# Performance work log

Measured on AMD Instinct MI355X. Metric: run time of the kernel, lower is better.

Reference implementation:

```python
import jax, jax.numpy as jnp
import numpy as np

B, C, H, W = 4, 256, 64, 64
CI = C // 2
EPS = 1e-5


def setup_inputs() -> dict:
    key = jax.random.key(0)
    ks = jax.random.split(key, 3)
    return {
        "x": jax.random.normal(ks[0], (B, C, H, W), dtype=jnp.float32) * 0.1,
        "g_w": jax.random.normal(ks[1], (CI, C), dtype=jnp.float32) * 0.05,
        "g_b": jnp.zeros((CI,), dtype=jnp.float32),
        "W_w": jax.random.normal(ks[2], (C, CI), dtype=jnp.float32) * 0.05,
        "W_b": jnp.zeros((C,), dtype=jnp.float32),
        "gamma": jnp.ones((C,), dtype=jnp.float32),
        "beta": jnp.zeros((C,), dtype=jnp.float32),
    }


def reference(x, g_w, g_b, W_w, W_b, gamma, beta):
    b, c, h, w = x.shape
    n = h * w
    ci = g_w.shape[0]
    # g: 1x1 conv C -> C/2
    g_x = jnp.einsum('oc,bchw->bohw', g_w, x) + g_b[None, :, None, None]
    g_x = g_x.reshape(b, ci, n).transpose(0, 2, 1)          # [B, N, Ci]
    theta = x.reshape(b, c, n).transpose(0, 2, 1)           # [B, N, C]
    phi = x.reshape(b, c, n)                                # [B, C, N]
    f = jnp.einsum('bnc,bcm->bnm', theta, phi)              # [B, N, N]
    attn = jax.nn.softmax(f, axis=-1)
    y = jnp.einsum('bnm,bmc->bnc', attn, g_x)               # [B, N, Ci]
    y = y.transpose(0, 2, 1).reshape(b, ci, h, w)
    # W: 1x1 conv C/2 -> C, then BatchNorm2d (training-mode batch stats)
    wy = jnp.einsum('oc,bchw->bohw', W_w, y) + W_b[None, :, None, None]
    mean = wy.mean(axis=(0, 2, 3))
    var = wy.var(axis=(0, 2, 3))  # biased, as torch BN uses for normalization
    wy = (wy - mean[None, :, None, None]) * jax.lax.rsqrt(var[None, :, None, None] + EPS)
    wy = wy * gamma[None, :, None, None] + beta[None, :, None, None]
    return wy + x
```

## Files before the change

kernel.cpp:

```cpp
#include <hip/hip_runtime.h>
#include <math.h>

#define B_ 4
#define C_ 256
#define CI_ 128
#define N_ 4096
#define QT_ 128
#define KT_ 64
#define KH_ 2048
#define NITER (KH_ / KT_)
#define KSTRIDE 264
#define VSTRIDE 72
constexpr float EPS_ = 1e-5f;

typedef __attribute__((ext_vector_type(8))) short bfrag;
typedef __attribute__((ext_vector_type(4))) float f4;

__device__ __forceinline__ unsigned short bf16r(float x) {
    unsigned u = __float_as_uint(x);
    u += 0x7FFFu + ((u >> 16) & 1u);
    return (unsigned short)(u >> 16);
}
__device__ __forceinline__ unsigned pack_bf16(float a, float b) {
    unsigned ua = __float_as_uint(a); ua += 0x7FFFu + ((ua >> 16) & 1u);
    unsigned ub = __float_as_uint(b); ub += 0x7FFFu + ((ub >> 16) & 1u);
    return (ua >> 16) | (ub & 0xFFFF0000u);
}

__global__ __launch_bounds__(256) void make_xt(const float* __restrict__ x,
                                               unsigned short* __restrict__ xt,
                                               float* __restrict__ sums) {
    if (blockIdx.x == 0 && blockIdx.y == 0 && blockIdx.z == 0) {
        sums[threadIdx.x] = 0.f;
        sums[threadIdx.x + 256] = 0.f;
    }
    int n  = blockIdx.x * 256 + threadIdx.x;
    int c0 = blockIdx.y * 8;
    int b  = blockIdx.z;
    const float* xb = x + (size_t)b * C_ * N_;
    unsigned short buf[8];
#pragma unroll
    for (int c = 0; c < 8; c++) buf[c] = bf16r(xb[(c0 + c) * N_ + n]);
    uint4 v;
    v.x = buf[0] | ((unsigned)buf[1] << 16);
    v.y = buf[2] | ((unsigned)buf[3] << 16);
    v.z = buf[4] | ((unsigned)buf[5] << 16);
    v.w = buf[6] | ((unsigned)buf[7] << 16);
    *(uint4*)&xt[((size_t)b * N_ + n) * C_ + c0] = v;
}

__global__ __launch_bounds__(256) void gconv(const float* __restrict__ x,
                                             const float* __restrict__ gw,
                                             const float* __restrict__ gb,
                                             unsigned short* __restrict__ gx) {
    int m  = blockIdx.x * 256 + threadIdx.x;
    int o0 = blockIdx.y * 16;
    int b  = blockIdx.z;
    const float* xb = x + (size_t)b * C_ * N_;
    float acc[16];
#pragma unroll
    for (int o = 0; o < 16; o++) acc[o] = gb[o0 + o];
    for (int c0 = 0; c0 < C_; c0 += 8) {
        float xv[8];
#pragma unroll
        for (int j = 0; j < 8; j++) xv[j] = xb[(c0 + j) * N_ + m];
#pragma unroll
        for (int o = 0; o < 16; o++) {
            const float* wr = gw + (size_t)(o0 + o) * C_ + c0;
#pragma unroll
            for (int j = 0; j < 8; j++) acc[o] += wr[j] * xv[j];
        }
    }
#pragma unroll
    for (int o = 0; o < 16; o++)
        gx[((size_t)b * CI_ + o0 + o) * N_ + m] = bf16r(acc[o]);
}

__global__ __launch_bounds__(1024, 4) void attn(const unsigned short* __restrict__ xt,
                                                const unsigned short* __restrict__ gx,
                                                float* __restrict__ Yp,
                                                float* __restrict__ ml) {
    __shared__ __align__(16) unsigned short Ks[2][64 * KSTRIDE];
    __shared__ __align__(16) unsigned short Vs[2][128 * VSTRIDE];
    __shared__ __align__(16) unsigned short Ps[128 * VSTRIDE];

    const int tid  = threadIdx.x;
    const int lane = tid & 63, w = tid >> 6;
    const int wq = w & 7, g = w >> 3;
    const int quad = lane >> 4, ql = lane & 15;
    const int half = blockIdx.x & 1;
    const int b    = (blockIdx.x & 7) >> 1;
    const int qt   = blockIdx.x >> 3;
    const int n0   = qt * QT_;
    const int kbase = half * KH_;
    const unsigned short* xtb = xt + (size_t)b * N_ * C_;
    const unsigned short* gxb = gx + (size_t)b * CI_ * N_;

    bfrag qb[8];
#pragma unroll
    for (int ks = 0; ks < 8; ks++)
        qb[ks] = *(const bfrag*)(xtb + (size_t)(n0 + 16 * wq + ql) * C_ + 32 * ks + quad * 8);

    f4 yacc[8];
    const f4 zero4 = {0.f, 0.f, 0.f, 0.f};
#pragma unroll
    for (int i = 0; i < 8; i++) yacc[i] = zero4;
    float mrun = -INFINITY, lrun = 0.f;

    uint4 kreg[2], vreg[1];
#pragma unroll
    for (int r = 0; r < 2; r++) {
        int idx = r * 1024 + tid;
        kreg[r] = *(const uint4*)(xtb + (size_t)(kbase + (idx >> 5)) * C_ + (idx & 31) * 8);
    }
    vreg[0] = *(const uint4*)(gxb + (size_t)(tid >> 3) * N_ + kbase + (tid & 7) * 8);
#pragma unroll
    for (int r = 0; r < 2; r++) {
        int idx = r * 1024 + tid;
        *(uint4*)&Ks[0][(idx >> 5) * KSTRIDE + (idx & 31) * 8] = kreg[r];
    }
    *(uint4*)&Vs[0][(tid >> 3) * VSTRIDE + (tid & 7) * 8] = vreg[0];
#pragma unroll
    for (int r = 0; r < 2; r++) {
        int idx = r * 1024 + tid;
        kreg[r] = *(const uint4*)(xtb + (size_t)(kbase + KT_ + (idx >> 5)) * C_ + (idx & 31) * 8);
    }
    vreg[0] = *(const uint4*)(gxb + (size_t)(tid >> 3) * N_ + kbase + KT_ + (tid & 7) * 8);
    __syncthreads();

    for (int it = 0; it < NITER; ++it) {
        const int cur = it & 1, nxt = cur ^ 1;

        if (it + 1 < NITER) {
#pragma unroll
            for (int r = 0; r < 2; r++) {
                int idx = r * 1024 + tid;
                *(uint4*)&Ks[nxt][(idx >> 5) * KSTRIDE + (idx & 31) * 8] = kreg[r];
            }
            *(uint4*)&Vs[nxt][(tid >> 3) * VSTRIDE + (tid & 7) * 8] = vreg[0];
        }
        if (it + 2 < NITER) {
            const int t0 = kbase + (it + 2) * KT_;
#pragma unroll
            for (int r = 0; r < 2; r++) {
                int idx = r * 1024 + tid;
                kreg[r] = *(const uint4*)(xtb + (size_t)(t0 + (idx >> 5)) * C_ + (idx & 31) * 8);
            }
            vreg[0] = *(const uint4*)(gxb + (size_t)(tid >> 3) * N_ + t0 + (tid & 7) * 8);
        }

        f4 sacc[2];
        sacc[0] = zero4; sacc[1] = zero4;
#pragma unroll
        for (int ks = 0; ks < 8; ks++) {
            bfrag ka[2];
#pragma unroll
            for (int i = 0; i < 2; i++)
                ka[i] = *(const bfrag*)&Ks[cur][(32 * g + 16 * i + ql) * KSTRIDE + 32 * ks + quad * 8];
#pragma unroll
            for (int i = 0; i < 2; i++)
                sacc[i] = __builtin_amdgcn_mfma_f32_16x16x32_bf16(ka[i], qb[ks], sacc[i], 0, 0, 0);
        }

        float mx = -INFINITY;
#pragma unroll
        for (int i = 0; i < 2; i++)
#pragma unroll
            for (int r = 0; r < 4; r++) mx = fmaxf(mx, sacc[i][r]);
        mx = fmaxf(mx, __shfl_xor(mx, 16, 64));
        mx = fmaxf(mx, __shfl_xor(mx, 32, 64));
        float mn = fmaxf(mrun, mx);
        float alpha = __expf(mrun - mn);
        mrun = mn;
        lrun *= alpha;
        if (__any(alpha != 1.f)) {
#pragma unroll
            for (int i = 0; i < 8; i++) {
                yacc[i][0] *= alpha; yacc[i][1] *= alpha;
                yacc[i][2] *= alpha; yacc[i][3] *= alpha;
            }
        }

        {
            int q = 16 * wq + ql;
            float lsum = 0.f;
#pragma unroll
            for (int i = 0; i < 2; i++) {
                float p0 = __expf(sacc[i][0] - mrun);
                float p1 = __expf(sacc[i][1] - mrun);
                float p2 = __expf(sacc[i][2] - mrun);
                float p3 = __expf(sacc[i][3] - mrun);
                lsum += (p0 + p1) + (p2 + p3);
                int idx = q * VSTRIDE + 32 * g + 16 * i + 4 * quad;
                unsigned long long pv = (unsigned long long)pack_bf16(p0, p1)
                                      | ((unsigned long long)pack_bf16(p2, p3) << 32);
                *(unsigned long long*)&Ps[idx] = pv;
            }
            lrun += lsum;
        }

        {
            bfrag pb, va[8];
            pb = *(const bfrag*)&Ps[(16 * wq + ql) * VSTRIDE + 32 * g + quad * 8];
#pragma unroll
            for (int i = 0; i < 8; i++)
                va[i] = *(const bfrag*)&Vs[cur][(16 * i + ql) * VSTRIDE + 32 * g + quad * 8];
#pragma unroll
            for (int i = 0; i < 8; i++)
                yacc[i] = __builtin_amdgcn_mfma_f32_16x16x32_bf16(va[i], pb, yacc[i], 0, 0, 0);
        }

        __syncthreads();
    }

    lrun += __shfl_xor(lrun, 16, 64);
    lrun += __shfl_xor(lrun, 32, 64);

    float* PsF = (float*)Ps;
    float* Ysc = PsF;
    float* mlb = PsF + 4096;

    const int q = 16 * wq + ql;
    if (quad == 0) {
        mlb[(g * 128 + q) * 2]     = mrun;
        mlb[(g * 128 + q) * 2 + 1] = lrun;
    }
    __syncthreads();
    float m0 = mlb[q * 2],           l0 = mlb[q * 2 + 1];
    float m1 = mlb[(128 + q) * 2],   l1 = mlb[(128 + q) * 2 + 1];
    float mm = fmaxf(m0, m1);
    float e0 = __expf(m0 - mm), e1 = __expf(m1 - mm);
    float lnew = e0 * l0 + e1 * l1;

#pragma unroll
    for (int c = 0; c < 4; c++) {
        if (g == 1) {
#pragma unroll
            for (int i2 = 0; i2 < 2; i2++) {
                int i = 2 * c + i2;
#pragma unroll
                for (int r = 0; r < 4; r++) {
                    int cip = 16 * i2 + 4 * quad + r;
                    Ysc[cip * 128 + q] = e1 * yacc[i][r];
                }
            }
        }
        __syncthreads();
        if (g == 0) {
#pragma unroll
            for (int i2 = 0; i2 < 2; i2++) {
                int i = 2 * c + i2;
#pragma unroll
                for (int r = 0; r < 4; r++) {
                    int ci = 16 * i + 4 * quad + r;
                    float v = e0 * yacc[i][r] + Ysc[(16 * i2 + 4 * quad + r) * 128 + q];
                    Yp[(((size_t)half * 4 + b) * CI_ + ci) * N_ + n0 + q] = v;
                }
            }
        }
        __syncthreads();
    }
    if (g == 0 && quad == 0) {
        ml[(((size_t)half * 4 + b) * N_ + n0 + q) * 2]     = mm;
        ml[(((size_t)half * 4 + b) * N_ + n0 + q) * 2 + 1] = lnew;
    }
}

__global__ __launch_bounds__(256) void wconv_stats(const float* __restrict__ Yp,
                                                   const float* __restrict__ ml,
                                                   const float* __restrict__ Ww,
                                                   const float* __restrict__ Wb,
                                                   float* __restrict__ wy,
                                                   float* __restrict__ sums) {
    int n   = blockIdx.x * 256 + threadIdx.x;
    int co0 = blockIdx.y * 16;
    int b   = blockIdx.z;

    float2 a0 = *(const float2*)&ml[((size_t)b * N_ + n) * 2];
    float2 a1 = *(const float2*)&ml[(((size_t)4 + b) * N_ + n) * 2];
    float mm = fmaxf(a0.x, a1.x);
    float e0 = __expf(a0.x - mm), e1 = __expf(a1.x - mm);
    float inv = 1.f / (e0 * a0.y + e1 * a1.y);
    float w0 = e0 * inv, w1 = e1 * inv;

    const float* y0b = Yp + (size_t)b * CI_ * N_;
    const float* y1b = Yp + (size_t)(4 + b) * CI_ * N_;
    float acc[16];
#pragma unroll
    for (int o = 0; o < 16; o++) acc[o] = Wb[co0 + o];
    for (int c0 = 0; c0 < CI_; c0 += 8) {
        float yv[8];
#pragma unroll
        for (int j = 0; j < 8; j++)
            yv[j] = w0 * y0b[(c0 + j) * N_ + n] + w1 * y1b[(c0 + j) * N_ + n];
#pragma unroll
        for (int o = 0; o < 16; o++) {
            const float* wr = Ww + (size_t)(co0 + o) * CI_ + c0;
#pragma unroll
            for (int j = 0; j < 8; j++) acc[o] += wr[j] * yv[j];
        }
    }
    float* wyb = wy + (size_t)b * C_ * N_;
#pragma unroll
    for (int o = 0; o < 16; o++) wyb[(co0 + o) * N_ + n] = acc[o];

    __shared__ float wred[32][4];
    int lane = threadIdx.x & 63, wid = threadIdx.x >> 6;
#pragma unroll
    for (int o = 0; o < 16; o++) {
        float s1 = acc[o], s2 = acc[o] * acc[o];
#pragma unroll
        for (int off = 32; off > 0; off >>= 1) {
            s1 += __shfl_down(s1, off, 64);
            s2 += __shfl_down(s2, off, 64);
        }
        if (lane == 0) { wred[o][wid] = s1; wred[16 + o][wid] = s2; }
    }
    __syncthreads();
    if (threadIdx.x < 32) {
        int qq = threadIdx.x;
        float t = wred[qq][0] + wred[qq][1] + wred[qq][2] + wred[qq][3];
        int o = qq & 15;
        if (qq < 16) atomicAdd(&sums[co0 + o], t);
        else         atomicAdd(&sums[256 + co0 + o], t);
    }
}

__global__ __launch_bounds__(256) void bn_finalize(float* __restrict__ wy,
                                                   const float* __restrict__ x,
                                                   const float* __restrict__ sums,
                                                   const float* __restrict__ gamma,
                                                   const float* __restrict__ beta,
                                                   float* __restrict__ out) {
    int n4 = blockIdx.x * 256 + threadIdx.x;
    int co = blockIdx.y;
    int b  = blockIdx.z;
    float cnt  = (float)(B_ * N_);
    float mean = sums[co] / cnt;
    float var  = sums[256 + co] / cnt - mean * mean;
    float sc   = rsqrtf(var + EPS_) * gamma[co];
    float bt   = beta[co];
    size_t idx = ((size_t)b * C_ + co) * N_ + (size_t)n4 * 4;
    float4 wv = *(const float4*)&wy[idx];
    float4 xv = *(const float4*)&x[idx];
    float4 o;
    o.x = (wv.x - mean) * sc + bt + xv.x;
    o.y = (wv.y - mean) * sc + bt + xv.y;
    o.z = (wv.z - mean) * sc + bt + xv.z;
    o.w = (wv.w - mean) * sc + bt + xv.w;
    *(float4*)&out[idx] = o;
}

extern "C" void kernel_launch(void* const* d_in, const int* in_sizes, int n_in,
                              void* d_out, int out_size, void* d_ws, size_t ws_size,
                              hipStream_t stream) {
    const float* x     = (const float*)d_in[0];
    const float* gw    = (const float*)d_in[1];
    const float* gb    = (const float*)d_in[2];
    const float* Ww    = (const float*)d_in[3];
    const float* Wb    = (const float*)d_in[4];
    const float* gamma = (const float*)d_in[5];
    const float* beta  = (const float*)d_in[6];
    float* out = (float*)d_out;
    float* ws  = (float*)d_ws;

    unsigned short* xt  = (unsigned short*)ws;
    unsigned short* gxb = (unsigned short*)(ws + 2097152);
    float* Yp   = ws + 3145728;
    float* ml   = ws + 7340032;
    float* sums = ws + 7405568;
    float* wy   = out;

    hipLaunchKernelGGL(make_xt, dim3(16, 32, 4), dim3(256), 0, stream, x, xt, sums);
    hipLaunchKernelGGL(gconv, dim3(16, 8, 4), dim3(256), 0, stream, x, gw, gb, gxb);
    hipLaunchKernelGGL(attn, dim3(256), dim3(1024), 0, stream, xt, gxb, Yp, ml);
    hipLaunchKernelGGL(wconv_stats, dim3(16, 16, 4), dim3(256), 0, stream, Yp, ml, Ww, Wb, wy, sums);
    hipLaunchKernelGGL(bn_finalize, dim3(4, 256, 4), dim3(256), 0, stream, wy, x, sums, gamma, beta, out);
}
```

Measured before the change: 275.7 us.

## Fuse transpose with g-conv and stage Y tile in LDS for W-conv

```diff
diff --git a/kernel.cpp b/kernel.cpp
--- a/kernel.cpp
+++ b/kernel.cpp
@@ -27,43 +27,49 @@
     return (ua >> 16) | (ub & 0xFFFF0000u);
 }
 
-__global__ __launch_bounds__(256) void make_xt(const float* __restrict__ x,
-                                               unsigned short* __restrict__ xt,
-                                               float* __restrict__ sums) {
-    if (blockIdx.x == 0 && blockIdx.y == 0 && blockIdx.z == 0) {
-        sums[threadIdx.x] = 0.f;
-        sums[threadIdx.x + 256] = 0.f;
-    }
-    int n  = blockIdx.x * 256 + threadIdx.x;
-    int c0 = blockIdx.y * 8;
-    int b  = blockIdx.z;
+__global__ __launch_bounds__(512) void gconv_xt(const float* __restrict__ x,
+                                                const float* __restrict__ gw,
+                                                const float* __restrict__ gb,
+                                                unsigned short* __restrict__ xt,
+                                                unsigned short* __restrict__ gx,
+                                                float* __restrict__ sums) {
+    __shared__ float xs[C_][65];
+    const int t = threadIdx.x, l = t & 63, w = t >> 6;
+    const int n0 = blockIdx.x * 64, b = blockIdx.y;
+    if (blockIdx.x == 0 && b == 0) sums[t] = 0.f;
+
     const float* xb = x + (size_t)b * C_ * N_;
-    unsigned short buf[8];
-#pragma unroll
-    for (int c = 0; c < 8; c++) buf[c] = bf16r(xb[(c0 + c) * N_ + n]);
-    uint4 v;
-    v.x = buf[0] | ((unsigned)buf[1] << 16);
-    v.y = buf[2] | ((unsigned)buf[3] << 16);
-    v.z = buf[4] | ((unsigned)buf[5] << 16);
-    v.w = buf[6] | ((unsigned)buf[7] << 16);
-    *(uint4*)&xt[((size_t)b * N_ + n) * C_ + c0] = v;
-}
-
-__global__ __launch_bounds__(256) void gconv(const float* __restrict__ x,
-                                             const float* __restrict__ gw,
-                                             const float* __restrict__ gb,
-                                             unsigned short* __restrict__ gx) {
-    int m  = blockIdx.x * 256 + threadIdx.x;
-    int o0 = blockIdx.y * 16;
-    int b  = blockIdx.z;
-    const float* xb = x + (size_t)b * C_ * N_;
+#pragma unroll
+    for (int k = 0; k < 32; k++) {
+        int c = 8 * k + w;
+        xs[c][l] = xb[(size_t)c * N_ + n0 + l];
+    }
+    __syncthreads();
+
+    {
+        unsigned short row[32];
+#pragma unroll
+        for (int j = 0; j < 32; j++) row[j] = bf16r(xs[32 * w + j][l]);
+        uint4* dst = (uint4*)&xt[((size_t)b * N_ + n0 + l) * C_ + 32 * w];
+#pragma unroll
+        for (int v = 0; v < 4; v++) {
+            uint4 u;
+            u.x = row[8 * v + 0] | ((unsigned)row[8 * v + 1] << 16);
+            u.y = row[8 * v + 2] | ((unsigned)row[8 * v + 3] << 16);
+            u.z = row[8 * v + 4] | ((unsigned)row[8 * v + 5] << 16);
+            u.w = row[8 * v + 6] | ((unsigned)row[8 * v + 7] << 16);
+            dst[v] = u;
+        }
+    }
+
+    const int o0 = 16 * w;
     float acc[16];
 #pragma unroll
     for (int o = 0; o < 16; o++) acc[o] = gb[o0 + o];
     for (int c0 = 0; c0 < C_; c0 += 8) {
         float xv[8];
 #pragma unroll
-        for (int j = 0; j < 8; j++) xv[j] = xb[(c0 + j) * N_ + m];
+        for (int j = 0; j < 8; j++) xv[j] = xs[c0 + j][l];
 #pragma unroll
         for (int o = 0; o < 16; o++) {
             const float* wr = gw + (size_t)(o0 + o) * C_ + c0;
@@ -73,7 +79,7 @@
     }
 #pragma unroll
     for (int o = 0; o < 16; o++)
-        gx[((size_t)b * CI_ + o0 + o) * N_ + m] = bf16r(acc[o]);
+        gx[((size_t)b * CI_ + o0 + o) * N_ + n0 + l] = bf16r(acc[o]);
 }
 
 __global__ __launch_bounds__(1024, 4) void attn(const unsigned short* __restrict__ xt,
@@ -266,15 +272,16 @@
     }
 }
 
-__global__ __launch_bounds__(256) void wconv_stats(const float* __restrict__ Yp,
+__global__ __launch_bounds__(512) void wconv_stats(const float* __restrict__ Yp,
                                                    const float* __restrict__ ml,
                                                    const float* __restrict__ Ww,
                                                    const float* __restrict__ Wb,
                                                    float* __restrict__ wy,
                                                    float* __restrict__ sums) {
-    int n   = blockIdx.x * 256 + threadIdx.x;
-    int co0 = blockIdx.y * 16;
-    int b   = blockIdx.z;
+    __shared__ float ys[CI_][66];
+    const int t = threadIdx.x, l = t & 63, w = t >> 6;
+    const int n0 = blockIdx.x * 64, b = blockIdx.y;
+    const int n = n0 + l;
 
     float2 a0 = *(const float2*)&ml[((size_t)b * N_ + n) * 2];
     float2 a1 = *(const float2*)&ml[(((size_t)4 + b) * N_ + n) * 2];
@@ -285,44 +292,48 @@
 
     const float* y0b = Yp + (size_t)b * CI_ * N_;
     const float* y1b = Yp + (size_t)(4 + b) * CI_ * N_;
-    float acc[16];
-#pragma unroll
-    for (int o = 0; o < 16; o++) acc[o] = Wb[co0 + o];
-    for (int c0 = 0; c0 < CI_; c0 += 8) {
-        float yv[8];
-#pragma unroll
-        for (int j = 0; j < 8; j++)
-            yv[j] = w0 * y0b[(c0 + j) * N_ + n] + w1 * y1b[(c0 + j) * N_ + n];
+#pragma unroll
+    for (int k = 0; k < 16; k++) {
+        int ci = 8 * k + w;
+        ys[ci][l] = w0 * y0b[(size_t)ci * N_ + n] + w1 * y1b[(size_t)ci * N_ + n];
+    }
+    __syncthreads();
+
+    float yv[CI_];
+#pragma unroll
+    for (int ci = 0; ci < CI_; ci++) yv[ci] = ys[ci][l];
+
+    float* wyb = wy + (size_t)b * C_ * N_;
+#pragma unroll
+    for (int ch = 0; ch < 2; ch++) {
+        const int co0 = 128 * ch + 16 * w;
+        float acc[16];
+#pragma unroll
+        for (int o = 0; o < 16; o++) acc[o] = Wb[co0 + o];
+        for (int c0 = 0; c0 < CI_; c0 += 8) {
+#pragma unroll
+            for (int o = 0; o < 16; o++) {
+                const float* wr = Ww + (size_t)(co0 + o) * CI_ + c0;
+#pragma unroll
+                for (int j = 0; j < 8; j++) acc[o] += wr[j] * yv[c0 + j];
+            }
+        }
+#pragma unroll
+        for (int o = 0; o < 16; o++) wyb[(size_t)(co0 + o) * N_ + n] = acc[o];
+
 #pragma unroll
         for (int o = 0; o < 16; o++) {
-            const float* wr = Ww + (size_t)(co0 + o) * CI_ + c0;
-#pragma unroll
-            for (int j = 0; j < 8; j++) acc[o] += wr[j] * yv[j];
-        }
-    }
-    float* wyb = wy + (size_t)b * C_ * N_;
-#pragma unroll
-    for (int o = 0; o < 16; o++) wyb[(co0 + o) * N_ + n] = acc[o];
-
-    __shared__ float wred[32][4];
-    int lane = threadIdx.x & 63, wid = threadIdx.x >> 6;
-#pragma unroll
-    for (int o = 0; o < 16; o++) {
-        float s1 = acc[o], s2 = acc[o] * acc[o];
-#pragma unroll
-        for (int off = 32; off > 0; off >>= 1) {
-            s1 += __shfl_down(s1, off, 64);
-            s2 += __shfl_down(s2, off, 64);
-        }
-        if (lane == 0) { wred[o][wid] = s1; wred[16 + o][wid] = s2; }
-    }
-    __syncthreads();
-    if (threadIdx.x < 32) {
-        int qq = threadIdx.x;
-        float t = wred[qq][0] + wred[qq][1] + wred[qq][2] + wred[qq][3];
-        int o = qq & 15;
-        if (qq < 16) atomicAdd(&sums[co0 + o], t);
-        else         atomicAdd(&sums[256 + co0 + o], t);
+            float s1 = acc[o], s2 = acc[o] * acc[o];
+#pragma unroll
+            for (int off = 32; off > 0; off >>= 1) {
+                s1 += __shfl_down(s1, off, 64);
+                s2 += __shfl_down(s2, off, 64);
+            }
+            if (l == 0) {
+                atomicAdd(&sums[co0 + o], s1);
+                atomicAdd(&sums[256 + co0 + o], s2);
+            }
+        }
     }
 }
 
@@ -371,9 +382,8 @@
     float* sums = ws + 7405568;
     float* wy   = out;
 
-    hipLaunchKernelGGL(make_xt, dim3(16, 32, 4), dim3(256), 0, stream, x, xt, sums);
-    hipLaunchKernelGGL(gconv, dim3(16, 8, 4), dim3(256), 0, stream, x, gw, gb, gxb);
+    hipLaunchKernelGGL(gconv_xt, dim3(64, 4), dim3(512), 0, stream, x, gw, gb, xt, gxb, sums);
     hipLaunchKernelGGL(attn, dim3(256), dim3(1024), 0, stream, xt, gxb, Yp, ml);
-    hipLaunchKernelGGL(wconv_stats, dim3(16, 16, 4), dim3(256), 0, stream, Yp, ml, Ww, Wb, wy, sums);
+    hipLaunchKernelGGL(wconv_stats, dim3(64, 4), dim3(512), 0, stream, Yp, ml, Ww, Wb, wy, sums);
     hipLaunchKernelGGL(bn_finalize, dim3(4, 256, 4), dim3(256), 0, stream, wy, x, sums, gamma, beta, out);
 }
```

Result: slower. 594.5 us (+115.6%).
